# Kernel tuning notes

Measured on AMD Instinct MI355X. Metric: run time of the kernel, lower is better.

## Reference

```python
import jax, jax.numpy as jnp
import numpy as np
import math

B, D, E = 32768, 256, 8          # batch, feature dim (shape=[256]), num_steps experts
T_TOTAL = 1.0
H_STEP = T_TOTAL / E             # self.h
EIGMIN, EIGINIT, EIGMAX = -1.0, 0.0, 1.0
LOGIT_099 = math.log(0.99 / 0.01)


def setup_inputs() -> dict:
    key = jax.random.key(0)
    k_t, k_y, k_w1, k_w2 = jax.random.split(key, 4)
    std = 1.0 / math.sqrt(D)     # xavier-ish init for expert weights
    return {
        "t": jax.random.uniform(k_t, (B,), dtype=jnp.float32),            # times in [0, T)
        "y": jax.random.normal(k_y, (B, D), dtype=jnp.float32),
        "W1": jax.random.normal(k_w1, (E, D, D), dtype=jnp.float32) * std,
        "b1": jnp.zeros((E, D), dtype=jnp.float32),
        "W2": jax.random.normal(k_w2, (E, D, D), dtype=jnp.float32) * std,
        "b2": jnp.zeros((E, D), dtype=jnp.float32),
        "scales": jnp.full((1, D), LOGIT_099, dtype=jnp.float32),         # learn_scales=False init
        "shifta": jnp.asarray(LOGIT_099, dtype=jnp.float32),
        "shiftb": jnp.asarray(LOGIT_099, dtype=jnp.float32),
    }


def reference(t, y, W1, b1, W2, b2, scales, shifta, shiftb):
    # t2ind: clamp(int(t / h), max=E-1)
    ind = jnp.minimum((t / H_STEP).astype(jnp.int32), E - 1)            # [B]
    # per-sample dispatch to expert F[i] (2-layer MLP), grouped as masked
    # dense batched GEMMs per expert (E is a small fixed set)
    f = jnp.zeros_like(y)
    for e in range(E):
        h_e = jnp.tanh(jnp.einsum('bd,kd->bk', y, W1[e]) + b1[e])       # [B, D]
        f_e = jnp.einsum('bd,kd->bk', h_e, W2[e]) + b2[e]               # [B, D]
        f = jnp.where((ind == e)[:, None], f_e, f)
    # sigmoid-scale / affine-combine epilogue
    f = jax.nn.sigmoid(scales) * f
    a = EIGINIT + jax.nn.sigmoid(shifta) * (EIGMIN - EIGINIT)
    b = EIGINIT + jax.nn.sigmoid(shiftb) * (EIGMAX - EIGINIT)
    return 0.5 * ((b - a) * f + (a + b) * y)
```

## Files before the change

### kernel.cpp

```cpp
#include <hip/hip_runtime.h>

#define BATCH 32768
#define DIM   256
#define NEXP  8
#define MT    64
#define STRIDE 264

typedef __bf16 bf16x8 __attribute__((ext_vector_type(8)));
typedef __bf16 bf16x4 __attribute__((ext_vector_type(4)));
typedef float  f32x16 __attribute__((ext_vector_type(16)));

static __device__ __forceinline__ float sigmoid_f(float x) {
    return __builtin_amdgcn_rcpf(1.f + __expf(-x));
}
static __device__ __forceinline__ float tanh_f(float x) {
    return 1.f - 2.f * __builtin_amdgcn_rcpf(__expf(2.f * x) + 1.f);
}

__global__ void prep_kernel(const float* __restrict__ W1, const float* __restrict__ W2,
                            const float* __restrict__ t,
                            bf16x8* __restrict__ W1p, bf16x8* __restrict__ W2p,
                            int* __restrict__ cursor, int* __restrict__ idxb) {
    const int b = blockIdx.x;
    if (b < 256) {
        const int tid = b * 256 + threadIdx.x;
        const int kh  = tid & 1;
        const int ks  = (tid >> 1) & 15;
        const int col = (tid >> 5) & 255;
        const int e   = tid >> 13;
        const long src = (long)tid * 8;
        const float4 a0 = *(const float4*)(W1 + src);
        const float4 a1 = *(const float4*)(W1 + src + 4);
        const float4 c0 = *(const float4*)(W2 + src);
        const float4 c1 = *(const float4*)(W2 + src + 4);
        bf16x8 w1, w2;
        w1[0] = (__bf16)a0.x; w1[1] = (__bf16)a0.y; w1[2] = (__bf16)a0.z; w1[3] = (__bf16)a0.w;
        w1[4] = (__bf16)a1.x; w1[5] = (__bf16)a1.y; w1[6] = (__bf16)a1.z; w1[7] = (__bf16)a1.w;
        w2[0] = (__bf16)c0.x; w2[1] = (__bf16)c0.y; w2[2] = (__bf16)c0.z; w2[3] = (__bf16)c0.w;
        w2[4] = (__bf16)c1.x; w2[5] = (__bf16)c1.y; w2[6] = (__bf16)c1.z; w2[7] = (__bf16)c1.w;
        const int dst = (e << 13) | ((col >> 5) << 10) | (ks << 6) | (kh << 5) | (col & 31);
        W1p[dst] = w1;
        W2p[dst] = w2;
    } else {
        __shared__ int h[NEXP], base[NEXP];
        if (threadIdx.x < NEXP) h[threadIdx.x] = 0;
        __syncthreads();
        const int i = (b - 256) * 256 + threadIdx.x;
        const int e = min((int)(t[i] * 8.0f), NEXP - 1);
        const int lr = atomicAdd(&h[e], 1);
        __syncthreads();
        if (threadIdx.x < NEXP)
            base[threadIdx.x] = atomicAdd(&cursor[threadIdx.x], h[threadIdx.x]);
        __syncthreads();
        idxb[e * BATCH + base[e] + lr] = i;
    }
}

__global__ void __launch_bounds__(512, 4)
mlp_kernel(const float* __restrict__ y,
           const float* __restrict__ scales,
           const float* __restrict__ shifta,
           const float* __restrict__ shiftb,
           const float* __restrict__ b1,
           const float* __restrict__ b2,
           const bf16x8* __restrict__ W1p,
           const bf16x8* __restrict__ W2p,
           const int* __restrict__ cnt,
           const int* __restrict__ idxb,
           float* __restrict__ out) {
    __shared__ __bf16 ab[MT * STRIDE];
    __shared__ int rows[MT];

    const int tx   = threadIdx.x;
    const int wave = tx >> 6;
    const int lane = tx & 63;
    const int nl   = lane & 31;
    const int kh   = lane >> 5;
    const int ncol = wave * 32;

    int c[NEXP], tp[NEXP + 1];
    tp[0] = 0;
#pragma unroll
    for (int e = 0; e < NEXP; ++e) {
        c[e] = cnt[e];
        tp[e + 1] = tp[e] + ((c[e] + MT - 1) >> 6);
    }
    const int total = tp[NEXP];

    const float sa = sigmoid_f(shifta[0]);
    const float sb = sigmoid_f(shiftb[0]);
    const float av = -sa;
    const float bvv = sb;
    const float k1 = 0.5f * (bvv - av);
    const float k2 = 0.5f * (av + bvv);
    const bool needy = (k2 != 0.0f);

    for (int tile = blockIdx.x; tile < total; tile += gridDim.x) {
        int e = 0;
#pragma unroll
        for (int j = 0; j < NEXP; ++j) if (tile >= tp[j + 1]) e = j + 1;
        const int rbase = (tile - tp[e]) * MT;
        const int nrows = min(MT, c[e] - rbase);
        const int* idx_e = idxb + e * BATCH;

        __syncthreads();
#pragma unroll
        for (int pass = 0; pass < 8; ++pass) {
            const int r  = pass * 8 + wave;
            const int rr = min(r, nrows - 1);
            const int g  = idx_e[rbase + rr];
            if (lane == 0) rows[r] = (r < nrows) ? g : -1;
            const float4 v = *(const float4*)(y + (long)g * DIM + lane * 4);
            bf16x4 w;
            w[0] = (__bf16)v.x; w[1] = (__bf16)v.y; w[2] = (__bf16)v.z; w[3] = (__bf16)v.w;
            *(bf16x4*)(ab + r * STRIDE + lane * 4) = w;
        }
        __syncthreads();

        const __bf16* apt0 = ab + nl * STRIDE + kh * 8;
        const __bf16* apt1 = ab + (32 + nl) * STRIDE + kh * 8;

        const bf16x8* w1p = W1p + (e << 13) + (wave << 10) + lane;
        f32x16 acc[2] = {};
#pragma unroll
        for (int ks = 0; ks < 16; ++ks) {
            bf16x8 a0 = *(const bf16x8*)(apt0 + ks * 16);
            bf16x8 a1 = *(const bf16x8*)(apt1 + ks * 16);
            bf16x8 bb = w1p[ks << 6];
            acc[0] = __builtin_amdgcn_mfma_f32_32x32x16_bf16(a0, bb, acc[0], 0, 0, 0);
            acc[1] = __builtin_amdgcn_mfma_f32_32x32x16_bf16(a1, bb, acc[1], 0, 0, 0);
        }
        __syncthreads();

        {
            const int n = ncol + nl;
            const float b1v = b1[(e << 8) | n];
#pragma unroll
            for (int mi = 0; mi < 2; ++mi) {
#pragma unroll
                for (int r = 0; r < 16; ++r) {
                    const int row = mi * 32 + (r & 3) + ((r >> 2) << 3) + (kh << 2);
                    ab[row * STRIDE + n] = (__bf16)tanh_f(acc[mi][r] + b1v);
                }
            }
        }
        __syncthreads();

        const bf16x8* w2p = W2p + (e << 13) + (wave << 10) + lane;
        f32x16 acc2[2] = {};
#pragma unroll
        for (int ks = 0; ks < 16; ++ks) {
            bf16x8 a0 = *(const bf16x8*)(apt0 + ks * 16);
            bf16x8 a1 = *(const bf16x8*)(apt1 + ks * 16);
            bf16x8 bb = w2p[ks << 6];
            acc2[0] = __builtin_amdgcn_mfma_f32_32x32x16_bf16(a0, bb, acc2[0], 0, 0, 0);
            acc2[1] = __builtin_amdgcn_mfma_f32_32x32x16_bf16(a1, bb, acc2[1], 0, 0, 0);
        }

        {
            const int n = ncol + nl;
            const float c1  = k1 * sigmoid_f(scales[n]);
            const float b2v = b2[(e << 8) | n];
#pragma unroll
            for (int mi = 0; mi < 2; ++mi) {
#pragma unroll
                for (int r = 0; r < 16; ++r) {
                    const int row = mi * 32 + (r & 3) + ((r >> 2) << 3) + (kh << 2);
                    const int g = rows[row];
                    if (g >= 0) {
                        float res = c1 * (acc2[mi][r] + b2v);
                        if (needy) res += k2 * y[(long)g * DIM + n];
                        out[(long)g * DIM + n] = res;
                    }
                }
            }
        }
    }
}

extern "C" void kernel_launch(void* const* d_in, const int* in_sizes, int n_in,
                              void* d_out, int out_size, void* d_ws, size_t ws_size,
                              hipStream_t stream) {
    const float* t      = (const float*)d_in[0];
    const float* y      = (const float*)d_in[1];
    const float* W1     = (const float*)d_in[2];
    const float* b1     = (const float*)d_in[3];
    const float* W2     = (const float*)d_in[4];
    const float* b2     = (const float*)d_in[5];
    const float* scales = (const float*)d_in[6];
    const float* shifta = (const float*)d_in[7];
    const float* shiftb = (const float*)d_in[8];
    float* out = (float*)d_out;

    char* ws = (char*)d_ws;
    int* cursor = (int*)ws;
    int* idxb   = (int*)(ws + 256);
    bf16x8* W1p = (bf16x8*)(ws + 256 + NEXP * BATCH * 4);
    bf16x8* W2p = W1p + 65536;

    hipMemsetAsync(cursor, 0, 32, stream);
    prep_kernel<<<384, 256, 0, stream>>>(W1, W2, t, W1p, W2p, cursor, idxb);
    mlp_kernel<<<520, 512, 0, stream>>>(y, scales, shifta, shiftb, b1, b2,
                                        W1p, W2p, cursor, idxb, out);
}
```

Measured before the change: 130.7 us.

## Shrink row tiles to 16 and switch to 16x16x32 MFMA with separate hidden buffer

Reduces the per-tile row count from 64 to 16 and moves from 32x32x16 to 16x16x32 MFMA. Weights are re-packed in prep to match the new operand layout. Blocks drop to 256 threads with a larger grid, and each wave now covers 64 output columns. A separate hidden-activation buffer and double-buffered row indices remove two barriers per tile. The aim is finer load balancing across expert tiles with fewer syncs, at the cost of reloading weights from cache four times as often per row.

Result: slower. 165.3 us (+26.5%).

```diff
diff --git a/kernel.cpp b/kernel.cpp
--- a/kernel.cpp
+++ b/kernel.cpp
@@ -3,12 +3,12 @@
 #define BATCH 32768
 #define DIM   256
 #define NEXP  8
-#define MT    64
+#define MT    16
 #define STRIDE 264
 
 typedef __bf16 bf16x8 __attribute__((ext_vector_type(8)));
 typedef __bf16 bf16x4 __attribute__((ext_vector_type(4)));
-typedef float  f32x16 __attribute__((ext_vector_type(16)));
+typedef float  f32x4  __attribute__((ext_vector_type(4)));
 
 static __device__ __forceinline__ float sigmoid_f(float x) {
     return __builtin_amdgcn_rcpf(1.f + __expf(-x));
@@ -24,10 +24,13 @@
     const int b = blockIdx.x;
     if (b < 256) {
         const int tid = b * 256 + threadIdx.x;
-        const int kh  = tid & 1;
-        const int ks  = (tid >> 1) & 15;
+        const int k8  = tid & 31;
         const int col = (tid >> 5) & 255;
         const int e   = tid >> 13;
+        const int kc  = k8 >> 2;
+        const int kq  = k8 & 3;
+        const int n16 = col & 15;
+        const int nt  = col >> 4;
         const long src = (long)tid * 8;
         const float4 a0 = *(const float4*)(W1 + src);
         const float4 a1 = *(const float4*)(W1 + src + 4);
@@ -38,7 +41,7 @@
         w1[4] = (__bf16)a1.x; w1[5] = (__bf16)a1.y; w1[6] = (__bf16)a1.z; w1[7] = (__bf16)a1.w;
         w2[0] = (__bf16)c0.x; w2[1] = (__bf16)c0.y; w2[2] = (__bf16)c0.z; w2[3] = (__bf16)c0.w;
         w2[4] = (__bf16)c1.x; w2[5] = (__bf16)c1.y; w2[6] = (__bf16)c1.z; w2[7] = (__bf16)c1.w;
-        const int dst = (e << 13) | ((col >> 5) << 10) | (ks << 6) | (kh << 5) | (col & 31);
+        const int dst = (e << 13) | (nt << 9) | (kc << 6) | (kq << 4) | n16;
         W1p[dst] = w1;
         W2p[dst] = w2;
     } else {
@@ -56,7 +59,7 @@
     }
 }
 
-__global__ void __launch_bounds__(512, 4)
+__global__ void __launch_bounds__(256, 8)
 mlp_kernel(const float* __restrict__ y,
            const float* __restrict__ scales,
            const float* __restrict__ shifta,
@@ -69,21 +72,22 @@
            const int* __restrict__ idxb,
            float* __restrict__ out) {
     __shared__ __bf16 ab[MT * STRIDE];
-    __shared__ int rows[MT];
+    __shared__ __bf16 ht[MT * STRIDE];
+    __shared__ int rows[2][MT];
 
     const int tx   = threadIdx.x;
     const int wave = tx >> 6;
     const int lane = tx & 63;
-    const int nl   = lane & 31;
-    const int kh   = lane >> 5;
-    const int ncol = wave * 32;
+    const int n16  = lane & 15;
+    const int quad = lane >> 4;
+    const int ncol = wave * 64;
 
     int c[NEXP], tp[NEXP + 1];
     tp[0] = 0;
 #pragma unroll
     for (int e = 0; e < NEXP; ++e) {
         c[e] = cnt[e];
-        tp[e + 1] = tp[e] + ((c[e] + MT - 1) >> 6);
+        tp[e + 1] = tp[e] + ((c[e] + MT - 1) >> 4);
     }
     const int total = tp[NEXP];
 
@@ -95,7 +99,8 @@
     const float k2 = 0.5f * (av + bvv);
     const bool needy = (k2 != 0.0f);
 
-    for (int tile = blockIdx.x; tile < total; tile += gridDim.x) {
+    int cb = 0;
+    for (int tile = blockIdx.x; tile < total; tile += gridDim.x, cb ^= 1) {
         int e = 0;
 #pragma unroll
         for (int j = 0; j < NEXP; ++j) if (tile >= tp[j + 1]) e = j + 1;
@@ -103,13 +108,12 @@
         const int nrows = min(MT, c[e] - rbase);
         const int* idx_e = idxb + e * BATCH;
 
-        __syncthreads();
-#pragma unroll
-        for (int pass = 0; pass < 8; ++pass) {
-            const int r  = pass * 8 + wave;
+#pragma unroll
+        for (int pass = 0; pass < 4; ++pass) {
+            const int r  = pass * 4 + wave;
             const int rr = min(r, nrows - 1);
             const int g  = idx_e[rbase + rr];
-            if (lane == 0) rows[r] = (r < nrows) ? g : -1;
+            if (lane == 0) rows[cb][r] = (r < nrows) ? g : -1;
             const float4 v = *(const float4*)(y + (long)g * DIM + lane * 4);
             bf16x4 w;
             w[0] = (__bf16)v.x; w[1] = (__bf16)v.y; w[2] = (__bf16)v.z; w[3] = (__bf16)v.w;
@@ -117,61 +121,58 @@
         }
         __syncthreads();
 
-        const __bf16* apt0 = ab + nl * STRIDE + kh * 8;
-        const __bf16* apt1 = ab + (32 + nl) * STRIDE + kh * 8;
-
-        const bf16x8* w1p = W1p + (e << 13) + (wave << 10) + lane;
-        f32x16 acc[2] = {};
-#pragma unroll
-        for (int ks = 0; ks < 16; ++ks) {
-            bf16x8 a0 = *(const bf16x8*)(apt0 + ks * 16);
-            bf16x8 a1 = *(const bf16x8*)(apt1 + ks * 16);
-            bf16x8 bb = w1p[ks << 6];
-            acc[0] = __builtin_amdgcn_mfma_f32_32x32x16_bf16(a0, bb, acc[0], 0, 0, 0);
-            acc[1] = __builtin_amdgcn_mfma_f32_32x32x16_bf16(a1, bb, acc[1], 0, 0, 0);
-        }
-        __syncthreads();
-
-        {
-            const int n = ncol + nl;
+        const __bf16* apt = ab + n16 * STRIDE + quad * 8;
+
+        const bf16x8* w1p = W1p + (e << 13) + ((ncol >> 4) << 9) + (quad << 4) + n16;
+        f32x4 acc[4] = {};
+#pragma unroll
+        for (int kc = 0; kc < 8; ++kc) {
+            bf16x8 a = *(const bf16x8*)(apt + kc * 32);
+#pragma unroll
+            for (int ni = 0; ni < 4; ++ni) {
+                bf16x8 bb = w1p[(ni << 9) + (kc << 6)];
+                acc[ni] = __builtin_amdgcn_mfma_f32_16x16x32_bf16(a, bb, acc[ni], 0, 0, 0);
+            }
+        }
+
+#pragma unroll
+        for (int ni = 0; ni < 4; ++ni) {
+            const int n = ncol + ni * 16 + n16;
             const float b1v = b1[(e << 8) | n];
 #pragma unroll
-            for (int mi = 0; mi < 2; ++mi) {
-#pragma unroll
-                for (int r = 0; r < 16; ++r) {
-                    const int row = mi * 32 + (r & 3) + ((r >> 2) << 3) + (kh << 2);
-                    ab[row * STRIDE + n] = (__bf16)tanh_f(acc[mi][r] + b1v);
-                }
-            }
-        }
-        __syncthreads();
-
-        const bf16x8* w2p = W2p + (e << 13) + (wave << 10) + lane;
-        f32x16 acc2[2] = {};
-#pragma unroll
-        for (int ks = 0; ks < 16; ++ks) {
-            bf16x8 a0 = *(const bf16x8*)(apt0 + ks * 16);
-            bf16x8 a1 = *(const bf16x8*)(apt1 + ks * 16);
-            bf16x8 bb = w2p[ks << 6];
-            acc2[0] = __builtin_amdgcn_mfma_f32_32x32x16_bf16(a0, bb, acc2[0], 0, 0, 0);
-            acc2[1] = __builtin_amdgcn_mfma_f32_32x32x16_bf16(a1, bb, acc2[1], 0, 0, 0);
-        }
-
-        {
-            const int n = ncol + nl;
+            for (int r = 0; r < 4; ++r) {
+                const int row = quad * 4 + r;
+                ht[row * STRIDE + n] = (__bf16)tanh_f(acc[ni][r] + b1v);
+            }
+        }
+        __syncthreads();
+
+        const __bf16* apt2 = ht + n16 * STRIDE + quad * 8;
+        const bf16x8* w2p = W2p + (e << 13) + ((ncol >> 4) << 9) + (quad << 4) + n16;
+        f32x4 acc2[4] = {};
+#pragma unroll
+        for (int kc = 0; kc < 8; ++kc) {
+            bf16x8 a = *(const bf16x8*)(apt2 + kc * 32);
+#pragma unroll
+            for (int ni = 0; ni < 4; ++ni) {
+                bf16x8 bb = w2p[(ni << 9) + (kc << 6)];
+                acc2[ni] = __builtin_amdgcn_mfma_f32_16x16x32_bf16(a, bb, acc2[ni], 0, 0, 0);
+            }
+        }
+
+#pragma unroll
+        for (int ni = 0; ni < 4; ++ni) {
+            const int n = ncol + ni * 16 + n16;
             const float c1  = k1 * sigmoid_f(scales[n]);
             const float b2v = b2[(e << 8) | n];
 #pragma unroll
-            for (int mi = 0; mi < 2; ++mi) {
-#pragma unroll
-                for (int r = 0; r < 16; ++r) {
-                    const int row = mi * 32 + (r & 3) + ((r >> 2) << 3) + (kh << 2);
-                    const int g = rows[row];
-                    if (g >= 0) {
-                        float res = c1 * (acc2[mi][r] + b2v);
-                        if (needy) res += k2 * y[(long)g * DIM + n];
-                        out[(long)g * DIM + n] = res;
-                    }
+            for (int r = 0; r < 4; ++r) {
+                const int row = quad * 4 + r;
+                const int g = rows[cb][row];
+                if (g >= 0) {
+                    float res = c1 * (acc2[ni][r] + b2v);
+                    if (needy) res += k2 * y[(long)g * DIM + n];
+                    out[(long)g * DIM + n] = res;
                 }
             }
         }
@@ -200,6 +201,6 @@
 
     hipMemsetAsync(cursor, 0, 32, stream);
     prep_kernel<<<384, 256, 0, stream>>>(W1, W2, t, W1p, W2p, cursor, idxb);
-    mlp_kernel<<<520, 512, 0, stream>>>(y, scales, shifta, shiftb, b1, b2,
-                                        W1p, W2p, cursor, idxb, out);
-}
+    mlp_kernel<<<2056, 256, 0, stream>>>(y, scales, shifta, shiftb, b1, b2,
+                                         W1p, W2p, cursor, idxb, out);
+}
```
